# Optimization experiments

Measured on AMD Instinct MI355X. Metric: run time of the kernel, lower is better.

## Reference

```python
import jax, jax.numpy as jnp
import numpy as np

B, D_BYTES, R, S, NSEG, OUT_DIM = 8, 128, 4096, 32768, 1024, 512
D_BITS = 8 * D_BYTES  # 1024


def setup_inputs() -> dict:
    key = jax.random.key(0)
    ks = jax.random.split(key, 9)
    u8 = lambda k, shape: jax.random.randint(k, shape, 0, 256, dtype=jnp.int32).astype(jnp.uint8)
    Q = u8(ks[0], (B, D_BYTES))
    Q_ok = u8(ks[1], (B, D_BYTES))
    refs = u8(ks[2], (R, D_BYTES))
    ok_pos = u8(ks[3], (R, D_BYTES))
    ref2seg = jax.random.randint(ks[4], (S,), 0, R, dtype=jnp.int32)
    segments = jnp.sort(jax.random.randint(ks[5], (S,), 0, NSEG, dtype=jnp.int32))
    W_o = jax.random.normal(ks[6], (D_BITS, OUT_DIM), dtype=jnp.float32) * (1.0 / np.sqrt(D_BITS))
    b_o = jnp.zeros((OUT_DIM,), dtype=jnp.float32)
    return {"Q": Q, "Q_ok": Q_ok, "refs": refs, "ok_pos": ok_pos,
            "ref2seg": ref2seg, "segments": segments, "N": NSEG,
            "W_o": W_o, "b_o": b_o}


def reference(Q, Q_ok, refs, ok_pos, ref2seg, segments, N, W_o, b_o):
    # values: unpack packed reference bit-sequences once: (R, d_bits) uint8
    values = jnp.unpackbits(refs, axis=1)

    def per_query(q, q_ok):
        # popcount sequence similarity, normalized by non-gap overlap length
        ok = jnp.sum(jax.lax.population_count(jnp.bitwise_and(q_ok, ok_pos)), axis=1)      # (R,)
        match = jnp.sum(jax.lax.population_count(jnp.bitwise_and(q, refs)), axis=1)        # (R,)
        dists = match / ok                                                                  # (R,) float32
        # numerically-stable segment softmax over ragged neighborhoods
        applied = jnp.take(dists, ref2seg)                                                  # (S,)
        mx = jnp.take(jax.ops.segment_max(applied, segments, num_segments=N), segments)
        e = applied - mx
        norm = jnp.take(jnp.log(jax.ops.segment_sum(jnp.exp(e), segments, num_segments=N)), segments)
        scores = jnp.exp(e - norm)                                                          # (S,)
        # gather values along edges, weight, scatter-sum into segments
        av = jnp.take(values, ref2seg, axis=0) * scores[:, None]                            # (S, d_bits)
        return jax.ops.segment_sum(av, segments, num_segments=N)                            # (N, d_bits)

    V = jax.vmap(per_query)(Q, Q_ok)        # (B, N, d_bits)
    return V @ W_o + b_o                     # (B, N, out_dim)
```

## Files before the change

### kernel.cpp

```cpp
#include <hip/hip_runtime.h>

#define B_Q   8
#define DB    128
#define R_REF 4096
#define S_EDGE 32768
#define NSEG  1024
#define DBITS 1024
#define OUTD  512

#define NB_WCONV 128
#define NB_DIST 2048
#define NB_BOUNDS 4
#define TILE_E 256

typedef __bf16 bf16_t;
typedef bf16_t bf16x8 __attribute__((ext_vector_type(8)));
typedef float  f32x4  __attribute__((ext_vector_type(4)));
typedef unsigned int u32;

__device__ inline unsigned short f2bf(float f){
  unsigned int u = __builtin_bit_cast(unsigned int, f);
  u = (u + 0x7fffu + ((u >> 16) & 1u)) >> 16;
  return (unsigned short)u;
}

__device__ __forceinline__ void gl_lds16(const unsigned short* g, unsigned short* l){
  __builtin_amdgcn_global_load_lds((const __attribute__((address_space(1))) u32*)g,
                                   (__attribute__((address_space(3))) u32*)l, 16, 0, 0);
}

__global__ __launch_bounds__(256) void k_prep(const float* __restrict__ W,
                                              unsigned short* __restrict__ WT,
                                              const int* __restrict__ refs,
                                              const int* __restrict__ Q,
                                              const int* __restrict__ Qok,
                                              const int* __restrict__ okpos,
                                              float* __restrict__ distsT,
                                              const int* __restrict__ segments,
                                              int* __restrict__ segstart){
  __shared__ float tile[64][65];
  const int bid = blockIdx.x;
  const int tid = threadIdx.x;

  if (bid < NB_WCONV){
    const int k0 = (bid & 15) * 64, o0 = (bid >> 4) * 64;
    const int tr = tid >> 6, tc = tid & 63;
    #pragma unroll
    for (int i = 0; i < 16; ++i)
      tile[tr + i*4][tc] = W[(size_t)(k0 + tr + i*4) * OUTD + o0 + tc];
    __syncthreads();
    #pragma unroll
    for (int i = 0; i < 16; ++i)
      WT[(size_t)(o0 + tr + i*4) * DBITS + k0 + tc] = f2bf(tile[tc][tr + i*4]);
  } else if (bid < NB_WCONV + NB_DIST){
    const int w = tid >> 6, l = tid & 63;
    const int base = (bid - NB_WCONV) * 16 + w * 4;
    const int b = base >> 12;
    const int q0 = Q[b*DB + l],   q1 = Q[b*DB + 64 + l];
    const int a0 = Qok[b*DB + l], a1 = Qok[b*DB + 64 + l];
    #pragma unroll
    for (int i = 0; i < 4; ++i){
      int r = (base + i) & 4095;
      int f0 = refs[r*DB + l], f1 = refs[r*DB + 64 + l];
      int p0 = okpos[r*DB + l],p1 = okpos[r*DB + 64 + l];
      int m = __popc(q0 & f0) + __popc(q1 & f1);
      int o = __popc(a0 & p0) + __popc(a1 & p1);
      int v = m | (o << 16);
      #pragma unroll
      for (int off = 32; off; off >>= 1) v += __shfl_down(v, off);
      if (l == 0) distsT[r * 8 + b] = (float)(v & 0xffff) / (float)(v >> 16);
    }
  } else {
    int n = (bid - NB_WCONV - NB_DIST) * 256 + tid;
    int lo = 0, hi = S_EDGE;
    #pragma unroll 1
    while (lo < hi){ int mid = (lo + hi) >> 1; if (segments[mid] < n) lo = mid + 1; else hi = mid; }
    segstart[n] = lo;
    if (n == 0) segstart[NSEG] = S_EDGE;
  }
}

__global__ __launch_bounds__(256) void k_ugemm(const int* __restrict__ refs,
                                               const unsigned short* __restrict__ WT,
                                               unsigned short* __restrict__ U){
  __shared__ unsigned short AS[2 * 8192];
  __shared__ unsigned short BS[2 * 8192];
  const int tid = threadIdx.x;
  const int bid = blockIdx.x;
  const int tn = (bid & 7) * 64, tm = (bid >> 3) * 64;
  const int w = tid >> 6, l = tid & 63;
  const int wm = (w & 1) * 32, wn = (w >> 1) * 32;
  const int lr = l & 15, kq = l >> 4;

  f32x4 acc[2][2] = {};
  int cur = 0;

  #define STAGE_B(buf, K0)                                                                 \
    do {                                                                                   \
      _Pragma("unroll")                                                                    \
      for (int c = 0; c < 4; ++c){                                                         \
        int idx = c * 256 + tid;                                                           \
        int row = idx >> 4, ch = idx & 15;                                                 \
        int gch = ch ^ (row & 15);                                                         \
        gl_lds16(WT + (size_t)(tn + row) * DBITS + (K0) + gch*8,                           \
                 BS + (buf)*8192 + row*128 + ch*8);                                        \
      }                                                                                    \
    } while (0)

  #define STAGE_A(buf, K0)                                                                 \
    do {                                                                                   \
      int row = tid >> 2, j0 = (tid & 3) * 4;                                              \
      int4 rv = *(const int4*)(refs + (size_t)(tm + row) * DB + (K0)/8 + j0);              \
      const int rx = row & 15;                                                             \
      int vv[4] = {rv.x, rv.y, rv.z, rv.w};                                                \
      _Pragma("unroll")                                                                    \
      for (int j = 0; j < 4; ++j){                                                         \
        u32 v = (u32)vv[j];                                                                \
        uint4 o;                                                                           \
        u32* wp = (u32*)&o;                                                                \
        _Pragma("unroll")                                                                  \
        for (int i2 = 0; i2 < 4; ++i2){                                                    \
          u32 b0 = (v >> (7 - 2*i2)) & 1u;                                                 \
          u32 b1 = (v >> (6 - 2*i2)) & 1u;                                                 \
          wp[i2] = b0 * 0x3F80u | ((b1 * 0x3F80u) << 16);                                  \
        }                                                                                  \
        int lch = (j0 + j) ^ rx;                                                           \
        *(uint4*)(AS + (buf)*8192 + row*128 + lch*8) = o;                                  \
      }                                                                                    \
    } while (0)

  STAGE_B(0, 0);
  STAGE_A(0, 0);
  __syncthreads();

  for (int s = 0; s < 8; ++s){
    if (s < 7){ STAGE_B(cur ^ 1, (s + 1) * 128); STAGE_A(cur ^ 1, (s + 1) * 128); }
    #pragma unroll
    for (int kk = 0; kk < 4; ++kk){
      bf16x8 af[2], bfr[2];
      #pragma unroll
      for (int m = 0; m < 2; ++m){
        int row = wm + m*16 + lr;
        int ch  = (kk*4 + kq) ^ (row & 15);
        af[m] = __builtin_bit_cast(bf16x8, *(const uint4*)(AS + cur*8192 + row*128 + ch*8));
      }
      #pragma unroll
      for (int n = 0; n < 2; ++n){
        int row = wn + n*16 + lr;
        int ch  = (kk*4 + kq) ^ (row & 15);
        bfr[n] = __builtin_bit_cast(bf16x8, *(const uint4*)(BS + cur*8192 + row*128 + ch*8));
      }
      #pragma unroll
      for (int m = 0; m < 2; ++m)
        #pragma unroll
        for (int n = 0; n < 2; ++n)
          acc[m][n] = __builtin_amdgcn_mfma_f32_16x16x32_bf16(af[m], bfr[n], acc[m][n], 0, 0, 0);
    }
    __syncthreads();
    cur ^= 1;
  }
  #undef STAGE_A
  #undef STAGE_B

  #pragma unroll
  for (int n = 0; n < 2; ++n)
    #pragma unroll
    for (int m = 0; m < 2; ++m){
      int row = tm + wm + m*16 + kq*4;
      int col = tn + wn + n*16 + lr;
      #pragma unroll
      for (int q = 0; q < 4; ++q)
        U[(size_t)(row + q) * OUTD + col] = f2bf(acc[m][n][q]);
    }
}

__global__ __launch_bounds__(256) void k_scat(const float* __restrict__ distsT,
                                              const int* __restrict__ ref2seg,
                                              const int* __restrict__ segstart,
                                              const unsigned short* __restrict__ U,
                                              const float* __restrict__ bo,
                                              float* __restrict__ out){
  __shared__ float mbs[8], ibs[8];
  __shared__ float scl[TILE_E * 8];
  __shared__ int   rix[TILE_E];
  const int n = blockIdx.x;
  const int t = threadIdx.x;

  const int start = segstart[n], end = segstart[n + 1];

  const float b0c = bo[2*t], b1c = bo[2*t + 1];
  float* op = out + (size_t)n * OUTD + 2*t;

  if (start >= end){
    #pragma unroll
    for (int j = 0; j < 8; ++j){
      op[(size_t)j * NSEG * OUTD]     = b0c;
      op[(size_t)j * NSEG * OUTD + 1] = b1c;
    }
    return;
  }

  if (t < 64){
    const int sb = t >> 3, es = t & 7;
    float m = -1e30f, s = 0.f;
    for (int e = start + es; e < end; e += 8){
      float d = distsT[ref2seg[e] * 8 + sb];
      float mn = fmaxf(m, d);
      s = s * __expf(m - mn) + __expf(d - mn);
      m = mn;
    }
    #pragma unroll
    for (int msk = 1; msk < 8; msk <<= 1){
      float mo = __shfl_xor(m, msk), so = __shfl_xor(s, msk);
      float mn = fmaxf(m, mo);
      s = s * __expf(m - mn) + so * __expf(mo - mn);
      m = mn;
    }
    if (es == 0){ mbs[sb] = m; ibs[sb] = 1.0f / s; }
  }
  __syncthreads();

  float acc[8][2];
  #pragma unroll
  for (int j = 0; j < 8; ++j){ acc[j][0] = 0.f; acc[j][1] = 0.f; }

  for (int e0 = start; e0 < end; e0 += TILE_E){
    const int cnt = min(TILE_E, end - e0);
    for (int i = t; i < cnt * 8; i += 256){
      int e = e0 + (i >> 3), b = i & 7;
      int r = ref2seg[e];
      if (b == 0) rix[i >> 3] = r;
      scl[i] = __expf(distsT[r*8 + b] - mbs[b]) * ibs[b];
    }
    __syncthreads();

    #pragma unroll 4
    for (int e = 0; e < cnt; ++e){
      int r = rix[e];
      float4 s0 = *(const float4*)(scl + e*8);
      float4 s1 = *(const float4*)(scl + e*8 + 4);
      u32 uu = *(const u32*)(U + ((size_t)r << 9) + 2*t);
      float ux = __builtin_bit_cast(float, uu << 16);
      float uy = __builtin_bit_cast(float, uu & 0xffff0000u);
      float ss[8] = {s0.x, s0.y, s0.z, s0.w, s1.x, s1.y, s1.z, s1.w};
      #pragma unroll
      for (int j = 0; j < 8; ++j){
        acc[j][0] += ss[j] * ux;
        acc[j][1] += ss[j] * uy;
      }
    }
    __syncthreads();
  }

  #pragma unroll
  for (int j = 0; j < 8; ++j){
    op[(size_t)j * NSEG * OUTD]     = acc[j][0] + b0c;
    op[(size_t)j * NSEG * OUTD + 1] = acc[j][1] + b1c;
  }
}

extern "C" void kernel_launch(void* const* d_in, const int* in_sizes, int n_in,
                              void* d_out, int out_size, void* d_ws, size_t ws_size,
                              hipStream_t stream) {
  const int*   Q        = (const int*)d_in[0];
  const int*   Qok      = (const int*)d_in[1];
  const int*   refs     = (const int*)d_in[2];
  const int*   okpos    = (const int*)d_in[3];
  const int*   ref2seg  = (const int*)d_in[4];
  const int*   segments = (const int*)d_in[5];
  const float* W        = (const float*)d_in[7];
  const float* bo       = (const float*)d_in[8];
  float* out = (float*)d_out;

  char* ws = (char*)d_ws;
  unsigned short* WT       = (unsigned short*)ws;
  float*          distsT   = (float*)(ws + (1u<<20));
  int*            segstart = (int*)(ws + (1u<<20) + (160u<<10));
  unsigned short* U        = (unsigned short*)(ws + (11u<<20));

  k_prep <<<NB_WCONV + NB_DIST + NB_BOUNDS, 256, 0, stream>>>(W, WT, refs, Q, Qok, okpos,
                                                              distsT, segments, segstart);
  k_ugemm<<<R_REF/64 * (OUTD/64), 256, 0, stream>>>(refs, WT, U);
  k_scat <<<NSEG, 256, 0, stream>>>(distsT, ref2seg, segstart, U, bo, out);
}
```

Before: 42.46 us.

## Overlap A-tile global loads with MFMA, vectorize popcount loads, widen softmax stats

The GEMM kernel now issues the global load of the next A tile before the MFMA loop and does the bit-unpack LDS write after it, so load latency overlaps compute. The distance kernel reads Q, Q_ok, refs and ok_pos with int2 loads at contiguous addresses instead of two strided scalar loads. The segment softmax statistics now use all 256 threads, 32 lanes per query, instead of 64 threads with 8 lanes each. The cost is more live registers in the GEMM and longer shuffle reductions.

```diff
diff --git a/kernel.cpp b/kernel.cpp
--- a/kernel.cpp
+++ b/kernel.cpp
@@ -56,15 +56,15 @@
     const int w = tid >> 6, l = tid & 63;
     const int base = (bid - NB_WCONV) * 16 + w * 4;
     const int b = base >> 12;
-    const int q0 = Q[b*DB + l],   q1 = Q[b*DB + 64 + l];
-    const int a0 = Qok[b*DB + l], a1 = Qok[b*DB + 64 + l];
+    const int2 q = *(const int2*)(Q   + b*DB + 2*l);
+    const int2 a = *(const int2*)(Qok + b*DB + 2*l);
     #pragma unroll
     for (int i = 0; i < 4; ++i){
       int r = (base + i) & 4095;
-      int f0 = refs[r*DB + l], f1 = refs[r*DB + 64 + l];
-      int p0 = okpos[r*DB + l],p1 = okpos[r*DB + 64 + l];
-      int m = __popc(q0 & f0) + __popc(q1 & f1);
-      int o = __popc(a0 & p0) + __popc(a1 & p1);
+      int2 f = *(const int2*)(refs  + r*DB + 2*l);
+      int2 p = *(const int2*)(okpos + r*DB + 2*l);
+      int m = __popc(q.x & f.x) + __popc(q.y & f.y);
+      int o = __popc(a.x & p.x) + __popc(a.y & p.y);
       int v = m | (o << 16);
       #pragma unroll
       for (int off = 32; off; off >>= 1) v += __shfl_down(v, off);
@@ -91,6 +91,8 @@
   const int w = tid >> 6, l = tid & 63;
   const int wm = (w & 1) * 32, wn = (w >> 1) * 32;
   const int lr = l & 15, kq = l >> 4;
+  const int arow = tid >> 2, aj0 = (tid & 3) * 4;
+  const int arx = arow & 15;
 
   f32x4 acc[2][2] = {};
   int cur = 0;
@@ -107,11 +109,10 @@
       }                                                                                    \
     } while (0)
 
-  #define STAGE_A(buf, K0)                                                                 \
+  #define A_LOAD(K0) (*(const int4*)(refs + (size_t)(tm + arow) * DB + (K0)/8 + aj0))
+
+  #define A_WRITE(buf, rv)                                                                 \
     do {                                                                                   \
-      int row = tid >> 2, j0 = (tid & 3) * 4;                                              \
-      int4 rv = *(const int4*)(refs + (size_t)(tm + row) * DB + (K0)/8 + j0);              \
-      const int rx = row & 15;                                                             \
       int vv[4] = {rv.x, rv.y, rv.z, rv.w};                                                \
       _Pragma("unroll")                                                                    \
       for (int j = 0; j < 4; ++j){                                                         \
@@ -124,17 +125,24 @@
           u32 b1 = (v >> (6 - 2*i2)) & 1u;                                                 \
           wp[i2] = b0 * 0x3F80u | ((b1 * 0x3F80u) << 16);                                  \
         }                                                                                  \
-        int lch = (j0 + j) ^ rx;                                                           \
-        *(uint4*)(AS + (buf)*8192 + row*128 + lch*8) = o;                                  \
+        int lch = (aj0 + j) ^ arx;                                                         \
+        *(uint4*)(AS + (buf)*8192 + arow*128 + lch*8) = o;                                 \
       }                                                                                    \
     } while (0)
 
-  STAGE_B(0, 0);
-  STAGE_A(0, 0);
+  {
+    int4 rv0 = A_LOAD(0);
+    STAGE_B(0, 0);
+    A_WRITE(0, rv0);
+  }
   __syncthreads();
 
   for (int s = 0; s < 8; ++s){
-    if (s < 7){ STAGE_B(cur ^ 1, (s + 1) * 128); STAGE_A(cur ^ 1, (s + 1) * 128); }
+    int4 rvn;
+    if (s < 7){
+      rvn = A_LOAD((s + 1) * 128);
+      STAGE_B(cur ^ 1, (s + 1) * 128);
+    }
     #pragma unroll
     for (int kk = 0; kk < 4; ++kk){
       bf16x8 af[2], bfr[2];
@@ -156,10 +164,12 @@
         for (int n = 0; n < 2; ++n)
           acc[m][n] = __builtin_amdgcn_mfma_f32_16x16x32_bf16(af[m], bfr[n], acc[m][n], 0, 0, 0);
     }
+    if (s < 7) A_WRITE(cur ^ 1, rvn);
     __syncthreads();
     cur ^= 1;
   }
-  #undef STAGE_A
+  #undef A_LOAD
+  #undef A_WRITE
   #undef STAGE_B
 
   #pragma unroll
@@ -200,17 +210,18 @@
     return;
   }
 
-  if (t < 64){
-    const int sb = t >> 3, es = t & 7;
+  {
+    const int w = t >> 6, l = t & 63;
+    const int sb = 2*w + (l >> 5), es = l & 31;
     float m = -1e30f, s = 0.f;
-    for (int e = start + es; e < end; e += 8){
+    for (int e = start + es; e < end; e += 32){
       float d = distsT[ref2seg[e] * 8 + sb];
       float mn = fmaxf(m, d);
       s = s * __expf(m - mn) + __expf(d - mn);
       m = mn;
     }
     #pragma unroll
-    for (int msk = 1; msk < 8; msk <<= 1){
+    for (int msk = 1; msk < 32; msk <<= 1){
       float mo = __shfl_xor(m, msk), so = __shfl_xor(s, msk);
       float mn = fmaxf(m, mo);
       s = s * __expf(m - mn) + so * __expf(mo - mn);
```

Result: no change. 42.58 us (+0.3%).
